# Optimization experiments

Hardware: AMD Instinct MI355X
Metric: run time of the kernel (lower is better)

Reference implementation:

```python
import jax, jax.numpy as jnp
import numpy as np

# TTM config (matches init_kwargs)
IN_SHAPE = (15, 15, 15, 15)   # TTM_dims[0], prod = 50625 = vocab
OUT_SHAPE = (8, 8, 8, 8)      # TTM_dims[1], prod = 4096 = out_features
RANKS = (1, 32, 64, 32, 1)
ROW_DIM = IN_SHAPE[0] * IN_SHAPE[1]  # 225, first unravel axis


def setup_inputs() -> dict:
    key = jax.random.key(0)
    ks = jax.random.split(key, 5)
    import math
    order = 4
    target_sdv = 1.0
    Us = {}
    for i in range(order):
        r1, r2 = RANKS[i], RANKS[i + 1]
        n1, n2 = IN_SHAPE[i], OUT_SHAPE[i]
        Us[f"U{i}"] = (jax.random.normal(ks[i], (r1, n1, n2, r2), dtype=jnp.float32)
                        / math.sqrt(r2) * target_sdv ** (1.0 / order))
    x = jax.random.randint(ks[4], (2, 4096), 0, int(np.prod(IN_SHAPE)), dtype=jnp.int64)
    return {"x": x, **Us}


def reference(x, U0, U1, U2, U3):
    # Precompute the two merged factors (small, vocab-independent):
    # out1: (n1_0*n1_1, n2_0*n2_1, r2) ; out2: (r2, n1_2*n1_3, n2_2*n2_3)
    t1 = jnp.tensordot(U0, U1, axes=[[3], [0]])        # (1, 15, 8, 15, 8, 64)
    t1 = jnp.moveaxis(t1, 3, 2)                         # (1, 15, 15, 8, 8, 64)
    out1 = t1.reshape(IN_SHAPE[0] * IN_SHAPE[1], OUT_SHAPE[0] * OUT_SHAPE[1], RANKS[2])
    t2 = jnp.tensordot(U2, U3, axes=[[3], [0]])        # (64, 15, 8, 15, 8, 1)
    t2 = jnp.moveaxis(t2, 3, 2)                         # (64, 15, 15, 8, 8, 1)
    out2 = t2.reshape(RANKS[2], IN_SHAPE[2] * IN_SHAPE[3], OUT_SHAPE[2] * OUT_SHAPE[3])

    xshape = x.shape
    xf = x.reshape(-1)
    # unravel_index of token id over [225, 225]
    row0 = xf // ROW_DIM
    row1 = xf % ROW_DIM
    a = out1[row0]            # (B, O1, r2)
    b = out2[:, row1, :]      # (r2, B, O2)
    rows = jnp.einsum('abc,cad->abd', a, b)   # (B, O1, O2)
    rows = rows.reshape(rows.shape[0], -1)     # (B, out_features)
    return rows.reshape(*xshape, -1)           # (*x.shape, 4096)
```

## Files before the change

kernel.cpp:

```cpp
#include <hip/hip_runtime.h>
#include <hip/hip_bf16.h>
#include <stdint.h>


typedef __attribute__((ext_vector_type(8))) __bf16 bf16x8;
typedef __attribute__((ext_vector_type(4))) float f32x4;

__device__ inline unsigned short f2bf(float f) {
    union { float f; unsigned u; } v; v.f = f;
    unsigned u = v.u;
    return (unsigned short)((u + 0x7fffu + ((u >> 16) & 1u)) >> 16);
}

__global__ __launch_bounds__(1024) void build_tables(const float* __restrict__ U0,
                                                     const float* __restrict__ U1,
                                                     const float* __restrict__ U2,
                                                     const float* __restrict__ U3,
                                                     unsigned short* __restrict__ O1,
                                                     unsigned short* __restrict__ O2) {
    __shared__ float smem[8960];
    const int b = blockIdx.x;
    const int t = threadIdx.x;

    f32x4 acc = (f32x4){0.f, 0.f, 0.f, 0.f};

    if (b < 225) {
        float* su0 = smem;
        float* su1 = smem + 256;
        const int p = b;
        const int i0 = p / 15, i1 = p % 15;
        const int o0 = t >> 7;
        const int o1 = (t >> 4) & 7;
        const int cq = t & 15;

        if (t < 256) su0[t] = U0[i0 * 256 + t];

        for (int h = 0; h < 2; ++h) {
            __syncthreads();
#pragma unroll
            for (int i = 0; i < 8; ++i) {
                int j = t + i * 1024;
                int r1h = j >> 9, rem = j & 511;
                su1[j] = U1[((h * 16 + r1h) * 15 + i1) * 512 + rem];
            }
            __syncthreads();
#pragma unroll
            for (int r = 0; r < 16; ++r) {
                f32x4 bvec = *(const f32x4*)(su1 + r * 512 + o1 * 64 + cq * 4);
                acc += su0[o0 * 32 + h * 16 + r] * bvec;
            }
        }
        ushort4 s = { f2bf(acc[0]), f2bf(acc[1]), f2bf(acc[2]), f2bf(acc[3]) };
        *(ushort4*)(O1 + p * 4096 + t * 4) = s;
    } else {
        float* su3 = smem;
        float* su2 = smem + 256;
        const int q = b - 225;
        const int i2 = q / 15, i3 = q % 15;
        const int o2 = t >> 7;
        const int o3 = (t >> 4) & 7;
        const int cq = t & 15;

        if (t < 256) {
            int r3 = t >> 3, o3s = t & 7;
            su3[t] = U3[(r3 * 15 + i3) * 8 + o3s];
        }

        for (int h = 0; h < 2; ++h) {
            __syncthreads();
#pragma unroll
            for (int i = 0; i < 8; ++i) {
                int j = t + i * 1024;
                int c = j >> 7, o2s = (j >> 4) & 7, r3h = j & 15;
                su2[(o2s * 16 + r3h) * 68 + c] =
                    U2[((c * 15 + i2) * 8 + o2s) * 32 + h * 16 + r3h];
            }
            __syncthreads();
#pragma unroll
            for (int r = 0; r < 16; ++r) {
                f32x4 bvec = *(const f32x4*)(su2 + (o2 * 16 + r) * 68 + cq * 4);
                acc += su3[(h * 16 + r) * 8 + o3] * bvec;
            }
        }
        ushort4 s = { f2bf(acc[0]), f2bf(acc[1]), f2bf(acc[2]), f2bf(acc[3]) };
        *(ushort4*)(O2 + q * 4096 + t * 4) = s;
    }
}

__global__ __launch_bounds__(256) void ttm_main(const int* __restrict__ x,
                                                const unsigned short* __restrict__ O1,
                                                const unsigned short* __restrict__ O2,
                                                float* __restrict__ out, int ne) {
    __shared__ float lbuf[4][16 * 68];
    const int w = threadIdx.x >> 6;
    const int l = threadIdx.x & 63;
    const int e = blockIdx.x * 4 + w;
    if (e >= ne) return;

    const unsigned v = (unsigned)x[e];
    const unsigned row0 = v / 225u;
    const unsigned row1 = v - row0 * 225u;

    const int lr = l & 15;
    const int lk = l >> 4;

    const unsigned short* Yp = O1 + (size_t)row0 * 4096;
    const unsigned short* Xp = O2 + (size_t)row1 * 4096;

    bf16x8 Y[4][2], X[4][2];
#pragma unroll
    for (int mq = 0; mq < 4; ++mq)
#pragma unroll
        for (int h = 0; h < 2; ++h)
            Y[mq][h] = *(const bf16x8*)(Yp + (16 * mq + lr) * 64 + h * 32 + lk * 8);
#pragma unroll
    for (int nq = 0; nq < 4; ++nq)
#pragma unroll
        for (int h = 0; h < 2; ++h)
            X[nq][h] = *(const bf16x8*)(Xp + (16 * nq + lr) * 64 + h * 32 + lk * 8);

    float* Oe = out + (size_t)e * 4096;
    float* Lw = lbuf[w];

#pragma unroll
    for (int mq = 0; mq < 4; ++mq) {
        f32x4 acc[4];
#pragma unroll
        for (int nq = 0; nq < 4; ++nq) {
            acc[nq] = __builtin_amdgcn_mfma_f32_16x16x32_bf16(
                X[nq][0], Y[mq][0], (f32x4){0.f, 0.f, 0.f, 0.f}, 0, 0, 0);
            acc[nq] = __builtin_amdgcn_mfma_f32_16x16x32_bf16(
                X[nq][1], Y[mq][1], acc[nq], 0, 0, 0);
        }
#pragma unroll
        for (int nq = 0; nq < 4; ++nq)
            *(f32x4*)(Lw + lr * 68 + 16 * nq + 4 * lk) = acc[nq];

#pragma unroll
        for (int i = 0; i < 4; ++i) {
            int chunk = i * 64 + l;
            int row = chunk >> 4, colq = chunk & 15;
            f32x4 vv = *(const f32x4*)(Lw + row * 68 + colq * 4);
            __builtin_nontemporal_store(vv, (f32x4*)(Oe + 1024 * mq + chunk * 4));
        }
    }
}

extern "C" void kernel_launch(void* const* d_in, const int* in_sizes, int n_in,
                              void* d_out, int out_size, void* d_ws, size_t ws_size,
                              hipStream_t stream) {
    const int* x = (const int*)d_in[0];
    const float* U0 = (const float*)d_in[1];
    const float* U1 = (const float*)d_in[2];
    const float* U2 = (const float*)d_in[3];
    const float* U3 = (const float*)d_in[4];

    unsigned short* O1 = (unsigned short*)d_ws;
    unsigned short* O2 = O1 + 225 * 4096;

    const int ne = in_sizes[0];

    build_tables<<<450, 1024, 0, stream>>>(U0, U1, U2, U3, O1, O2);
    ttm_main<<<(ne + 3) / 4, 256, 0, stream>>>(x, O1, O2, (float*)d_out, ne);
}
```

Before: 40.95 us.

## Bucket tokens by first-factor row so each block reuses its O1 slice

The main kernel becomes 900 blocks, four per O1 row. Each block scans a quarter of the token ids, collects those whose row0 matches its row into a shared list, loads the O1 slice once, and loops over the matching tokens. This trades redundant O1 loads per token for every block scanning its share of x and an uneven number of tokens per block. The output stores also switch from nontemporal to ordinary stores. The hard-coded scan bound of 8192 tokens silently drops tokens if ne is larger.

Result: slower. 52.02 us (+27.1%).

```diff
diff --git a/kernel.cpp b/kernel.cpp
--- a/kernel.cpp
+++ b/kernel.cpp
@@ -87,61 +87,85 @@
     }
 }
 
-__global__ __launch_bounds__(256) void ttm_main(const int* __restrict__ x,
-                                                const unsigned short* __restrict__ O1,
-                                                const unsigned short* __restrict__ O2,
-                                                float* __restrict__ out, int ne) {
+__global__ __launch_bounds__(256) void ttm_bucketed(const int* __restrict__ x,
+                                                    const unsigned short* __restrict__ O1,
+                                                    const unsigned short* __restrict__ O2,
+                                                    float* __restrict__ out, int ne) {
+    __shared__ int list[2048];
+    __shared__ int cnt;
     __shared__ float lbuf[4][16 * 68];
-    const int w = threadIdx.x >> 6;
-    const int l = threadIdx.x & 63;
-    const int e = blockIdx.x * 4 + w;
-    if (e >= ne) return;
-
-    const unsigned v = (unsigned)x[e];
-    const unsigned row0 = v / 225u;
-    const unsigned row1 = v - row0 * 225u;
-
+    const int p = blockIdx.x >> 2;
+    const int s = blockIdx.x & 3;
+    const int t = threadIdx.x;
+    const int w = t >> 6;
+    const int l = t & 63;
     const int lr = l & 15;
     const int lk = l >> 4;
 
-    const unsigned short* Yp = O1 + (size_t)row0 * 4096;
-    const unsigned short* Xp = O2 + (size_t)row1 * 4096;
+    if (t == 0) cnt = 0;
+    __syncthreads();
 
-    bf16x8 Y[4][2], X[4][2];
+#pragma unroll
+    for (int i = 0; i < 8; ++i) {
+        int j = 4 * (t + 256 * i) + s;
+        if (j < ne) {
+            unsigned v = (unsigned)x[j];
+            if (v / 225u == (unsigned)p) {
+                int idx = atomicAdd(&cnt, 1);
+                list[idx] = j;
+            }
+        }
+    }
+    __syncthreads();
+    const int n = cnt;
+    if (n == 0) return;
+
+    const unsigned short* Yp = O1 + (size_t)p * 4096;
+    bf16x8 Y[4][2];
 #pragma unroll
     for (int mq = 0; mq < 4; ++mq)
 #pragma unroll
         for (int h = 0; h < 2; ++h)
             Y[mq][h] = *(const bf16x8*)(Yp + (16 * mq + lr) * 64 + h * 32 + lk * 8);
-#pragma unroll
-    for (int nq = 0; nq < 4; ++nq)
-#pragma unroll
-        for (int h = 0; h < 2; ++h)
-            X[nq][h] = *(const bf16x8*)(Xp + (16 * nq + lr) * 64 + h * 32 + lk * 8);
 
-    float* Oe = out + (size_t)e * 4096;
     float* Lw = lbuf[w];
 
-#pragma unroll
-    for (int mq = 0; mq < 4; ++mq) {
-        f32x4 acc[4];
-#pragma unroll
-        for (int nq = 0; nq < 4; ++nq) {
-            acc[nq] = __builtin_amdgcn_mfma_f32_16x16x32_bf16(
-                X[nq][0], Y[mq][0], (f32x4){0.f, 0.f, 0.f, 0.f}, 0, 0, 0);
-            acc[nq] = __builtin_amdgcn_mfma_f32_16x16x32_bf16(
-                X[nq][1], Y[mq][1], acc[nq], 0, 0, 0);
-        }
+    for (int i = w; i < n; i += 4) {
+        const int e = list[i];
+        const unsigned v = (unsigned)x[e];
+        const unsigned row1 = v - 225u * (unsigned)p;
+        const unsigned short* Xp = O2 + (size_t)row1 * 4096;
+
+        bf16x8 X[4][2];
 #pragma unroll
         for (int nq = 0; nq < 4; ++nq)
-            *(f32x4*)(Lw + lr * 68 + 16 * nq + 4 * lk) = acc[nq];
+#pragma unroll
+            for (int h = 0; h < 2; ++h)
+                X[nq][h] = *(const bf16x8*)(Xp + (16 * nq + lr) * 64 + h * 32 + lk * 8);
+
+        float* Oe = out + (size_t)e * 4096;
 
 #pragma unroll
-        for (int i = 0; i < 4; ++i) {
-            int chunk = i * 64 + l;
-            int row = chunk >> 4, colq = chunk & 15;
-            f32x4 vv = *(const f32x4*)(Lw + row * 68 + colq * 4);
-            __builtin_nontemporal_store(vv, (f32x4*)(Oe + 1024 * mq + chunk * 4));
+        for (int mq = 0; mq < 4; ++mq) {
+            f32x4 acc[4];
+#pragma unroll
+            for (int nq = 0; nq < 4; ++nq) {
+                acc[nq] = __builtin_amdgcn_mfma_f32_16x16x32_bf16(
+                    X[nq][0], Y[mq][0], (f32x4){0.f, 0.f, 0.f, 0.f}, 0, 0, 0);
+                acc[nq] = __builtin_amdgcn_mfma_f32_16x16x32_bf16(
+                    X[nq][1], Y[mq][1], acc[nq], 0, 0, 0);
+            }
+#pragma unroll
+            for (int nq = 0; nq < 4; ++nq)
+                *(f32x4*)(Lw + lr * 68 + 16 * nq + 4 * lk) = acc[nq];
+
+#pragma unroll
+            for (int ii = 0; ii < 4; ++ii) {
+                int chunk = ii * 64 + l;
+                int row = chunk >> 4, colq = chunk & 15;
+                f32x4 vv = *(const f32x4*)(Lw + row * 68 + colq * 4);
+                *(f32x4*)(Oe + 1024 * mq + chunk * 4) = vv;
+            }
         }
     }
 }
@@ -161,5 +185,5 @@
     const int ne = in_sizes[0];
 
     build_tables<<<450, 1024, 0, stream>>>(U0, U1, U2, U3, O1, O2);
-    ttm_main<<<(ne + 3) / 4, 256, 0, stream>>>(x, O1, O2, (float*)d_out, ne);
+    ttm_bucketed<<<225 * 4, 256, 0, stream>>>(x, O1, O2, (float*)d_out, ne);
 }
```

## Sort tokens by O2 row and map blocks to contiguous sorted chunks per XCD

Applied to the files above, without the earlier changes.

An extra block in the table-build kernel counting-sorts token indices by row1 (v % 225) into a permutation buffer. The main kernel reads tokens through this permutation and maps blocks round-robin so each of the 8 XCDs handles a contiguous slice of sorted tokens. The aim is to improve L2 reuse of O2 table rows within each XCD. In exchange, one block does a serial histogram and scatter that can lengthen the build kernel. The slot indexing assumes ne is divisible by 8, otherwise some tokens are skipped.

New measurement: 44.96 us. 9.8% more time.

```diff
diff --git a/kernel.cpp b/kernel.cpp
--- a/kernel.cpp
+++ b/kernel.cpp
@@ -17,10 +17,34 @@
                                                      const float* __restrict__ U2,
                                                      const float* __restrict__ U3,
                                                      unsigned short* __restrict__ O1,
-                                                     unsigned short* __restrict__ O2) {
+                                                     unsigned short* __restrict__ O2,
+                                                     const int* __restrict__ x,
+                                                     int* __restrict__ perm, int ne) {
     __shared__ float smem[8960];
     const int b = blockIdx.x;
     const int t = threadIdx.x;
+
+    if (b == 450) {
+        __shared__ int hist[225];
+        if (t < 225) hist[t] = 0;
+        __syncthreads();
+        for (int j = t; j < ne; j += 1024) {
+            unsigned v = (unsigned)x[j];
+            atomicAdd(&hist[v % 225u], 1);
+        }
+        __syncthreads();
+        if (t == 0) {
+            int s = 0;
+            for (int i = 0; i < 225; ++i) { int c = hist[i]; hist[i] = s; s += c; }
+        }
+        __syncthreads();
+        for (int j = t; j < ne; j += 1024) {
+            unsigned v = (unsigned)x[j];
+            int pos = atomicAdd(&hist[v % 225u], 1);
+            perm[pos] = j;
+        }
+        return;
+    }
 
     f32x4 acc = (f32x4){0.f, 0.f, 0.f, 0.f};
 
@@ -88,14 +112,18 @@
 }
 
 __global__ __launch_bounds__(256) void ttm_main(const int* __restrict__ x,
+                                                const int* __restrict__ perm,
                                                 const unsigned short* __restrict__ O1,
                                                 const unsigned short* __restrict__ O2,
                                                 float* __restrict__ out, int ne) {
     __shared__ float lbuf[4][16 * 68];
+    const int b = blockIdx.x;
     const int w = threadIdx.x >> 6;
     const int l = threadIdx.x & 63;
-    const int e = blockIdx.x * 4 + w;
-    if (e >= ne) return;
+    const int nper = ne >> 3;
+    const int slot = (b & 7) * nper + (b >> 3) * 4 + w;
+    if (slot >= ne) return;
+    const int e = perm[slot];
 
     const unsigned v = (unsigned)x[e];
     const unsigned row0 = v / 225u;
@@ -157,9 +185,10 @@
 
     unsigned short* O1 = (unsigned short*)d_ws;
     unsigned short* O2 = O1 + 225 * 4096;
+    int* perm = (int*)(O2 + 225 * 4096);
 
     const int ne = in_sizes[0];
 
-    build_tables<<<450, 1024, 0, stream>>>(U0, U1, U2, U3, O1, O2);
-    ttm_main<<<(ne + 3) / 4, 256, 0, stream>>>(x, O1, O2, (float*)d_out, ne);
+    build_tables<<<451, 1024, 0, stream>>>(U0, U1, U2, U3, O1, O2, x, perm, ne);
+    ttm_main<<<(ne + 3) / 4, 256, 0, stream>>>(x, perm, O1, O2, (float*)d_out, ne);
 }
```
